# Kernel tuning notes

Hardware: AMD Instinct MI355X
Metric: run time of the kernel (lower is better)

Reference implementation:

```python
import jax, jax.numpy as jnp
import numpy as np

NUM_SPINS = 1024
BATCH = 4096
INPUT_DIM = 2
NUM_HIDDEN = 128
NUM_LAYERS = 1
FIXED_MAG = 0


def setup_inputs() -> dict:
    key = jax.random.key(0)
    ks = jax.random.split(key, 7)
    # spins one-hot encoded, as the module's masking math assumes
    spins = jax.random.randint(ks[0], (NUM_SPINS, BATCH), 0, 2)
    data_in = jax.nn.one_hot(spins, INPUT_DIM, dtype=jnp.float32)
    s = 1.0 / np.sqrt(NUM_HIDDEN)  # torch RNNCell default uniform bound
    W_ih = jax.random.uniform(ks[1], (NUM_HIDDEN, INPUT_DIM), minval=-s, maxval=s, dtype=jnp.float32)
    W_hh = jax.random.uniform(ks[2], (NUM_HIDDEN, NUM_HIDDEN), minval=-s, maxval=s, dtype=jnp.float32)
    b_ih = jax.random.uniform(ks[3], (NUM_HIDDEN,), minval=-s, maxval=s, dtype=jnp.float32)
    b_hh = jax.random.uniform(ks[4], (NUM_HIDDEN,), minval=-s, maxval=s, dtype=jnp.float32)
    W_lin = jax.random.uniform(ks[5], (INPUT_DIM, NUM_HIDDEN), minval=-s, maxval=s, dtype=jnp.float32)
    b_lin = jax.random.uniform(ks[6], (INPUT_DIM,), minval=-s, maxval=s, dtype=jnp.float32)
    return {"data_in": data_in, "W_ih": W_ih, "W_hh": W_hh,
            "b_ih": b_ih, "b_hh": b_hh, "W_lin": W_lin, "b_lin": b_lin}


def reference(data_in, W_ih, W_hh, b_ih, b_hh, W_lin, b_lin):
    S, B, I = data_in.shape
    dt = data_in.dtype
    # input sequence shifted by one spin, first input is init_state [1,0]
    init_state = jnp.array([1.0, 0.0], dtype=dt)
    data = jnp.concatenate([jnp.broadcast_to(init_state, (1, B, I)), data_in[:-1]], axis=0)

    def step(h, x):
        for _ in range(NUM_LAYERS):  # source re-applies the SAME cell num_layers times
            h = jnp.tanh(x @ W_ih.T + b_ih + h @ W_hh.T + b_hh)
        probs = jax.nn.softmax(h @ W_lin.T + b_lin, axis=-1)
        return h, probs

    h0 = jnp.zeros((B, NUM_HIDDEN), dtype=dt)
    _, state_probs = jax.lax.scan(step, h0, data)  # [S, B, I]

    # conditional masking from fixed magnetization
    half = S // 2
    thresh_up = half + (S % 2) + FIXED_MAG // 2
    thresh_down = half - FIXED_MAG // 2
    cum_up = jnp.cumsum(data_in[:, :, 0], axis=0)    # [S, B]
    cum_down = jnp.cumsum(data_in[:, :, 1], axis=0)  # [S, B]
    down_guar = jnp.array([0.0, 1.0], dtype=dt)
    up_guar = jnp.array([1.0, 0.0], dtype=dt)
    mask_up = (cum_up[:-1] >= thresh_up)[..., None]      # for spins 1..S-1
    mask_down = (cum_down[:-1] >= thresh_down)[..., None]
    corr = jnp.where(mask_up, down_guar, state_probs[1:])
    corr = jnp.where(mask_down, up_guar, corr)
    return jnp.concatenate([state_probs[:1], corr], axis=0)
```

## Files before the change

kernel.cpp:

```cpp
#include <hip/hip_runtime.h>

#define NS 1024
#define NB 4096
#define NH 128
#define RB 16
#define NT 512

typedef __attribute__((ext_vector_type(8))) short short8;
typedef __attribute__((ext_vector_type(4))) float f32x4;

__device__ __forceinline__ short f2bf(float x) {
    unsigned u = __builtin_bit_cast(unsigned, x);
    u = (u + 0x7FFFu + ((u >> 16) & 1u)) >> 16;
    return (short)u;
}
__device__ __forceinline__ float vexp2(float x) {
    float r;
    asm("v_exp_f32 %0, %1" : "=v"(r) : "v"(x));
    return r;
}

#define BARRIER() asm volatile("s_waitcnt lgkmcnt(0)\n\ts_barrier" ::: "memory")

__global__ __launch_bounds__(NT, 1)
void pwf_kernel(const float* __restrict__ data_in,
                const float* __restrict__ W_ih,
                const float* __restrict__ W_hh,
                const float* __restrict__ b_ih,
                const float* __restrict__ b_hh,
                const float* __restrict__ W_lin,
                const float* __restrict__ b_lin,
                float* __restrict__ out)
{
    __shared__ __align__(16) short hlds[2][RB * NH];
    __shared__ unsigned selm[2];
    __shared__ uint2    msk[4];

    const int tid = threadIdx.x;
    const int w   = tid >> 6;
    const int l   = tid & 63;
    const int g   = l >> 4;
    const int b   = l & 15;
    const int b0  = blockIdx.x * RB;

    const float TL2E = 2.8853900817779268f;
    const float L2E  = 1.4426950408889634f;

    const int hrow = w * 16 + b;
    short8 afrag[4];
    #pragma unroll
    for (int kb = 0; kb < 4; ++kb) {
        const float* src = W_hh + hrow * NH + kb * 32 + g * 8;
        short8 v;
        #pragma unroll
        for (int i = 0; i < 8; ++i) v[i] = f2bf(TL2E * src[i]);
        afrag[kb] = v;
    }
    short8 lfrag[4];
    #pragma unroll
    for (int kb = 0; kb < 4; ++kb) {
        short8 v;
        #pragma unroll
        for (int i = 0; i < 8; ++i) {
            const int k = kb * 32 + g * 8 + i;
            v[i] = (b == 0) ? f2bf(L2E * (W_lin[NH + k] - W_lin[k])) : (short)0;
        }
        lfrag[kb] = v;
    }

    float cv0[4], cv1[4];
    #pragma unroll
    for (int r = 0; r < 4; ++r) {
        const int hid = w * 16 + 4 * g + r;
        const float cb = b_ih[hid] + b_hh[hid];
        cv0[r] = TL2E * (W_ih[hid * 2 + 0] + cb);
        cv1[r] = TL2E * (W_ih[hid * 2 + 1] + cb);
    }
    const float blD = L2E * (b_lin[1] - b_lin[0]);

    int aoff[4];
    #pragma unroll
    for (int kb = 0; kb < 4; ++kb)
        aoff[kb] = b * NH + ((kb * 32 + g * 8 + 8 * b) & 127);
    const int woffs = b * NH + ((w * 16 + 4 * g + 8 * b) & 127);

    ((uint4*)hlds)[tid] = make_uint4(0u, 0u, 0u, 0u);
    if (tid == 0) { selm[0] = 0u; msk[0] = make_uint2(0u, 0u); }
    int cntup = 0, cntdn = 0;
    const int rr = (l < RB) ? l : (RB - 1);
    float suA = 0.0f, suB = 0.0f;
    if (w == 7) {
        suA = data_in[(size_t)(b0 + rr) * 2];
        suB = data_in[((size_t)NB + b0 + rr) * 2];
    }
    float ediff = 0.0f;
    unsigned eum = 0u, edm = 0u;
    BARRIER();

#define STEP(T, P, SU)                                                         \
    {                                                                          \
        const short* hr = hlds[P];                                             \
        short* hw = hlds[(P) ^ 1];                                             \
        const unsigned sel = selm[P];                                          \
        const short8 h0 = *(const short8*)&hr[aoff[0]];                        \
        const short8 h1 = *(const short8*)&hr[aoff[1]];                        \
        const short8 h2 = *(const short8*)&hr[aoff[2]];                        \
        const short8 h3 = *(const short8*)&hr[aoff[3]];                        \
        if (w == 0 && (T) >= 2 && l < 16) {       \
            float p0 = __builtin_amdgcn_rcpf(1.0f + vexp2(ediff));             \
            float p1 = 1.0f - p0;                                              \
            if ((eum >> l) & 1u) { p0 = 0.0f; p1 = 1.0f; }                     \
            if ((edm >> l) & 1u) { p0 = 1.0f; p1 = 0.0f; }                     \
            *(float2*)&out[((size_t)((T) - 2) * NB + b0 + l) * 2] =            \
                make_float2(p0, p1);                                           \
        }                                                                      \
                           \
        f32x4 zz = {0.f, 0.f, 0.f, 0.f};                                       \
        f32x4 c01 = __builtin_amdgcn_mfma_f32_16x16x32_bf16(afrag[0], h0, zz, 0, 0, 0); \
        c01 = __builtin_amdgcn_mfma_f32_16x16x32_bf16(afrag[1], h1, c01, 0, 0, 0); \
        f32x4 c23 = __builtin_amdgcn_mfma_f32_16x16x32_bf16(afrag[2], h2, zz, 0, 0, 0); \
        c23 = __builtin_amdgcn_mfma_f32_16x16x32_bf16(afrag[3], h3, c23, 0, 0, 0); \
        if (w == 0 && (T) >= 1) {                \
            f32x4 d01 = __builtin_amdgcn_mfma_f32_16x16x32_bf16(lfrag[0], h0, zz, 0, 0, 0); \
            d01 = __builtin_amdgcn_mfma_f32_16x16x32_bf16(lfrag[1], h1, d01, 0, 0, 0); \
            f32x4 d23 = __builtin_amdgcn_mfma_f32_16x16x32_bf16(lfrag[2], h2, zz, 0, 0, 0); \
            d23 = __builtin_amdgcn_mfma_f32_16x16x32_bf16(lfrag[3], h3, d23, 0, 0, 0); \
            ediff = d01[0] + d23[0] + blD;     \
            const uint2 mm = msk[((T) - 1) & 3];                               \
            eum = mm.x; edm = mm.y;                                            \
        }                                                                      \
        const unsigned sb = (sel >> b) & 1u;                                   \
        float hn[4];                                                           \
        _Pragma("unroll")                                                      \
        for (int r = 0; r < 4; ++r) {                                          \
            const float cv = sb ? cv1[r] : cv0[r];                             \
            const float e  = vexp2(c01[r] + c23[r] + cv);                      \
            hn[r] = fmaf(__builtin_amdgcn_rcpf(e + 1.0f), -2.0f, 1.0f);        \
        }                                                                      \
        unsigned pk01, pk23;                                                   \
        asm("v_cvt_pk_bf16_f32 %0, %1, %2" : "=v"(pk01) : "v"(hn[0]), "v"(hn[1])); \
        asm("v_cvt_pk_bf16_f32 %0, %1, %2" : "=v"(pk23) : "v"(hn[2]), "v"(hn[3])); \
        *(uint2*)&hw[woffs] = make_uint2(pk01, pk23);    \
        if (w == 7) {         \
            const int isup = ((SU) > 0.5f) ? 1 : 0;                            \
            cntup += isup; cntdn += 1 - isup;                                  \
            const unsigned long long bs = __ballot(l < RB && isup == 0);       \
            const unsigned long long bu = __ballot(l < RB && cntup >= NS / 2); \
            const unsigned long long bd = __ballot(l < RB && cntdn >= NS / 2); \
            if (l == 0) {                                                      \
                selm[(P) ^ 1] = (unsigned)bs & 0xFFFFu;                        \
                msk[((T) + 1) & 3] =                                           \
                    make_uint2((unsigned)bu & 0xFFFFu, (unsigned)bd & 0xFFFFu);\
            }                                                                  \
            const int tn = ((T) + 2 < NS) ? (T) + 2 : NS - 1;                  \
            (SU) = data_in[((size_t)tn * NB + b0 + rr) * 2];                   \
        }                                                                      \
        BARRIER();                                                             \
    }

    for (int t = 0; t < NS; t += 2) {
        STEP(t, 0, suA)
        STEP(t + 1, 1, suB)
    }

    if (w == 0) {
        if (l < 16) {
            float p0 = __builtin_amdgcn_rcpf(1.0f + vexp2(ediff));
            float p1 = 1.0f - p0;
            if ((eum >> l) & 1u) { p0 = 0.0f; p1 = 1.0f; }
            if ((edm >> l) & 1u) { p0 = 1.0f; p1 = 0.0f; }
            *(float2*)&out[((size_t)(NS - 2) * NB + b0 + l) * 2] =
                make_float2(p0, p1);
        }
        const short* hr = hlds[0];
        const short8 h0 = *(const short8*)&hr[aoff[0]];
        const short8 h1 = *(const short8*)&hr[aoff[1]];
        const short8 h2 = *(const short8*)&hr[aoff[2]];
        const short8 h3 = *(const short8*)&hr[aoff[3]];
        f32x4 zz = {0.f, 0.f, 0.f, 0.f};
        f32x4 d01 = __builtin_amdgcn_mfma_f32_16x16x32_bf16(lfrag[0], h0, zz, 0, 0, 0);
        d01 = __builtin_amdgcn_mfma_f32_16x16x32_bf16(lfrag[1], h1, d01, 0, 0, 0);
        f32x4 d23 = __builtin_amdgcn_mfma_f32_16x16x32_bf16(lfrag[2], h2, zz, 0, 0, 0);
        d23 = __builtin_amdgcn_mfma_f32_16x16x32_bf16(lfrag[3], h3, d23, 0, 0, 0);
        const float fdiff = d01[0] + d23[0] + blD;
        const uint2 mm = msk[(NS - 1) & 3];
        if (l < 16) {
            float p0 = __builtin_amdgcn_rcpf(1.0f + vexp2(fdiff));
            float p1 = 1.0f - p0;
            if ((mm.x >> l) & 1u) { p0 = 0.0f; p1 = 1.0f; }
            if ((mm.y >> l) & 1u) { p0 = 1.0f; p1 = 0.0f; }
            *(float2*)&out[((size_t)(NS - 1) * NB + b0 + l) * 2] =
                make_float2(p0, p1);
        }
    }
}

extern "C" void kernel_launch(void* const* d_in, const int* in_sizes, int n_in,
                              void* d_out, int out_size, void* d_ws, size_t ws_size,
                              hipStream_t stream) {
    const float* data_in = (const float*)d_in[0];
    const float* W_ih    = (const float*)d_in[1];
    const float* W_hh    = (const float*)d_in[2];
    const float* b_ih    = (const float*)d_in[3];
    const float* b_hh    = (const float*)d_in[4];
    const float* W_lin   = (const float*)d_in[5];
    const float* b_lin   = (const float*)d_in[6];
    float* out = (float*)d_out;

    dim3 grid(NB / RB);
    dim3 block(NT);
    pwf_kernel<<<grid, block, 0, stream>>>(data_in, W_ih, W_hh, b_ih, b_hh,
                                           W_lin, b_lin, out);
}
```

Before: 415.5 us.

## Halve batch rows per block and compute masks per-thread, removing LDS mask broadcast

Each block now handles 8 batch rows with 4 waves, and each wave computes two 16-row hidden tiles (X and Y halves) instead of one. This doubles the grid to 512 blocks and allows two blocks per CU. The magnetization counters and input-select bit are now tracked redundantly in every thread, which removes the LDS selm/msk broadcasts and the ballots. The output wave rotates across blocks and raises its priority while writing. In exchange, half of every MFMA is wasted because the 16-wide batch dimension is padded with duplicate rows, and each wave does twice the MFMA work per step.

```diff
diff --git a/kernel.cpp b/kernel.cpp
--- a/kernel.cpp
+++ b/kernel.cpp
@@ -3,8 +3,9 @@
 #define NS 1024
 #define NB 4096
 #define NH 128
-#define RB 16
-#define NT 512
+#define RB 8
+#define NT 256
+#define HLF (NS / 2)
 
 typedef __attribute__((ext_vector_type(8))) short short8;
 typedef __attribute__((ext_vector_type(4))) float f32x4;
@@ -22,7 +23,7 @@
 
 #define BARRIER() asm volatile("s_waitcnt lgkmcnt(0)\n\ts_barrier" ::: "memory")
 
-__global__ __launch_bounds__(NT, 1)
+__global__ __launch_bounds__(NT, 2)
 void pwf_kernel(const float* __restrict__ data_in,
                 const float* __restrict__ W_ih,
                 const float* __restrict__ W_hh,
@@ -33,28 +34,30 @@
                 float* __restrict__ out)
 {
     __shared__ __align__(16) short hlds[2][RB * NH];
-    __shared__ unsigned selm[2];
-    __shared__ uint2    msk[4];
 
     const int tid = threadIdx.x;
     const int w   = tid >> 6;
     const int l   = tid & 63;
     const int g   = l >> 4;
     const int b   = l & 15;
+    const int br  = b & 7;
     const int b0  = blockIdx.x * RB;
+    const int LW  = blockIdx.x & 3;
 
     const float TL2E = 2.8853900817779268f;
     const float L2E  = 1.4426950408889634f;
 
-    const int hrow = w * 16 + b;
-    short8 afrag[4];
+    const int hrX = w * 16 + b;
+    const int hrY = hrX + 64;
+    short8 aX[4], aY[4];
     #pragma unroll
     for (int kb = 0; kb < 4; ++kb) {
-        const float* src = W_hh + hrow * NH + kb * 32 + g * 8;
-        short8 v;
+        const float* sx = W_hh + hrX * NH + kb * 32 + g * 8;
+        const float* sy = W_hh + hrY * NH + kb * 32 + g * 8;
+        short8 vx, vy;
         #pragma unroll
-        for (int i = 0; i < 8; ++i) v[i] = f2bf(TL2E * src[i]);
-        afrag[kb] = v;
+        for (int i = 0; i < 8; ++i) { vx[i] = f2bf(TL2E * sx[i]); vy[i] = f2bf(TL2E * sy[i]); }
+        aX[kb] = vx; aY[kb] = vy;
     }
     short8 lfrag[4];
     #pragma unroll
@@ -68,93 +71,103 @@
         lfrag[kb] = v;
     }
 
-    float cv0[4], cv1[4];
+    float cvX0[4], cvX1[4], cvY0[4], cvY1[4];
     #pragma unroll
     for (int r = 0; r < 4; ++r) {
-        const int hid = w * 16 + 4 * g + r;
-        const float cb = b_ih[hid] + b_hh[hid];
-        cv0[r] = TL2E * (W_ih[hid * 2 + 0] + cb);
-        cv1[r] = TL2E * (W_ih[hid * 2 + 1] + cb);
+        const int hx = w * 16 + 4 * g + r;
+        const int hy = hx + 64;
+        const float cbx = b_ih[hx] + b_hh[hx];
+        const float cby = b_ih[hy] + b_hh[hy];
+        cvX0[r] = TL2E * (W_ih[hx * 2 + 0] + cbx);
+        cvX1[r] = TL2E * (W_ih[hx * 2 + 1] + cbx);
+        cvY0[r] = TL2E * (W_ih[hy * 2 + 0] + cby);
+        cvY1[r] = TL2E * (W_ih[hy * 2 + 1] + cby);
     }
     const float blD = L2E * (b_lin[1] - b_lin[0]);
 
     int aoff[4];
     #pragma unroll
     for (int kb = 0; kb < 4; ++kb)
-        aoff[kb] = b * NH + ((kb * 32 + g * 8 + 8 * b) & 127);
-    const int woffs = b * NH + ((w * 16 + 4 * g + 8 * b) & 127);
+        aoff[kb] = br * NH + ((kb * 32 + g * 8 + 8 * br) & 127);
+    const int woffX = br * NH + ((w * 16 + 4 * g + 8 * br) & 127);
+    const int woffY = br * NH + ((w * 16 + 64 + 4 * g + 8 * br) & 127);
 
     ((uint4*)hlds)[tid] = make_uint4(0u, 0u, 0u, 0u);
-    if (tid == 0) { selm[0] = 0u; msk[0] = make_uint2(0u, 0u); }
     int cntup = 0, cntdn = 0;
-    const int rr = (l < RB) ? l : (RB - 1);
-    float suA = 0.0f, suB = 0.0f;
-    if (w == 7) {
-        suA = data_in[(size_t)(b0 + rr) * 2];
-        suB = data_in[((size_t)NB + b0 + rr) * 2];
-    }
+    int selp = 0;
+    int ump = 0, dmp = 0;
+    float suA = data_in[(size_t)(b0 + br) * 2];
+    float suB = data_in[((size_t)NB + b0 + br) * 2];
     float ediff = 0.0f;
-    unsigned eum = 0u, edm = 0u;
+    int eum = 0, edm = 0;
     BARRIER();
 
 #define STEP(T, P, SU)                                                         \
     {                                                                          \
         const short* hr = hlds[P];                                             \
         short* hw = hlds[(P) ^ 1];                                             \
-        const unsigned sel = selm[P];                                          \
         const short8 h0 = *(const short8*)&hr[aoff[0]];                        \
         const short8 h1 = *(const short8*)&hr[aoff[1]];                        \
         const short8 h2 = *(const short8*)&hr[aoff[2]];                        \
         const short8 h3 = *(const short8*)&hr[aoff[3]];                        \
-        if (w == 0 && (T) >= 2 && l < 16) {       \
-            float p0 = __builtin_amdgcn_rcpf(1.0f + vexp2(ediff));             \
-            float p1 = 1.0f - p0;                                              \
-            if ((eum >> l) & 1u) { p0 = 0.0f; p1 = 1.0f; }                     \
-            if ((edm >> l) & 1u) { p0 = 1.0f; p1 = 0.0f; }                     \
-            *(float2*)&out[((size_t)((T) - 2) * NB + b0 + l) * 2] =            \
-                make_float2(p0, p1);                                           \
-        }                                                                      \
-                           \
+        if (w == LW) {                                                         \
+            __builtin_amdgcn_s_setprio(1);                                     \
+            if ((T) >= 2 && l < 8) {              \
+                float p0 = __builtin_amdgcn_rcpf(1.0f + vexp2(ediff));         \
+                float p1 = 1.0f - p0;                                          \
+                if (eum) { p0 = 0.0f; p1 = 1.0f; }                             \
+                if (edm) { p0 = 1.0f; p1 = 0.0f; }         \
+                *(float2*)&out[((size_t)((T) - 2) * NB + b0 + l) * 2] =        \
+                    make_float2(p0, p1);                                       \
+            }                                                                  \
+        }                                                                      \
+                \
         f32x4 zz = {0.f, 0.f, 0.f, 0.f};                                       \
-        f32x4 c01 = __builtin_amdgcn_mfma_f32_16x16x32_bf16(afrag[0], h0, zz, 0, 0, 0); \
-        c01 = __builtin_amdgcn_mfma_f32_16x16x32_bf16(afrag[1], h1, c01, 0, 0, 0); \
-        f32x4 c23 = __builtin_amdgcn_mfma_f32_16x16x32_bf16(afrag[2], h2, zz, 0, 0, 0); \
-        c23 = __builtin_amdgcn_mfma_f32_16x16x32_bf16(afrag[3], h3, c23, 0, 0, 0); \
-        if (w == 0 && (T) >= 1) {                \
+        f32x4 cX01 = __builtin_amdgcn_mfma_f32_16x16x32_bf16(aX[0], h0, zz, 0, 0, 0); \
+        cX01 = __builtin_amdgcn_mfma_f32_16x16x32_bf16(aX[1], h1, cX01, 0, 0, 0); \
+        f32x4 cX23 = __builtin_amdgcn_mfma_f32_16x16x32_bf16(aX[2], h2, zz, 0, 0, 0); \
+        cX23 = __builtin_amdgcn_mfma_f32_16x16x32_bf16(aX[3], h3, cX23, 0, 0, 0); \
+        f32x4 cY01 = __builtin_amdgcn_mfma_f32_16x16x32_bf16(aY[0], h0, zz, 0, 0, 0); \
+        cY01 = __builtin_amdgcn_mfma_f32_16x16x32_bf16(aY[1], h1, cY01, 0, 0, 0); \
+        f32x4 cY23 = __builtin_amdgcn_mfma_f32_16x16x32_bf16(aY[2], h2, zz, 0, 0, 0); \
+        cY23 = __builtin_amdgcn_mfma_f32_16x16x32_bf16(aY[3], h3, cY23, 0, 0, 0); \
+        if (w == LW && (T) >= 1) {               \
             f32x4 d01 = __builtin_amdgcn_mfma_f32_16x16x32_bf16(lfrag[0], h0, zz, 0, 0, 0); \
             d01 = __builtin_amdgcn_mfma_f32_16x16x32_bf16(lfrag[1], h1, d01, 0, 0, 0); \
             f32x4 d23 = __builtin_amdgcn_mfma_f32_16x16x32_bf16(lfrag[2], h2, zz, 0, 0, 0); \
             d23 = __builtin_amdgcn_mfma_f32_16x16x32_bf16(lfrag[3], h3, d23, 0, 0, 0); \
-            ediff = d01[0] + d23[0] + blD;     \
-            const uint2 mm = msk[((T) - 1) & 3];                               \
-            eum = mm.x; edm = mm.y;                                            \
-        }                                                                      \
-        const unsigned sb = (sel >> b) & 1u;                                   \
-        float hn[4];                                                           \
+            ediff = d01[0] + d23[0] + blD;            \
+            eum = ump; edm = dmp;                      \
+        }                                                                      \
+        ump = (cntup >= HLF);        \
+        dmp = (cntdn >= HLF);                                                  \
+        float hnX[4], hnY[4];                                                  \
         _Pragma("unroll")                                                      \
         for (int r = 0; r < 4; ++r) {                                          \
-            const float cv = sb ? cv1[r] : cv0[r];                             \
-            const float e  = vexp2(c01[r] + c23[r] + cv);                      \
-            hn[r] = fmaf(__builtin_amdgcn_rcpf(e + 1.0f), -2.0f, 1.0f);        \
-        }                                                                      \
-        unsigned pk01, pk23;                                                   \
-        asm("v_cvt_pk_bf16_f32 %0, %1, %2" : "=v"(pk01) : "v"(hn[0]), "v"(hn[1])); \
-        asm("v_cvt_pk_bf16_f32 %0, %1, %2" : "=v"(pk23) : "v"(hn[2]), "v"(hn[3])); \
-        *(uint2*)&hw[woffs] = make_uint2(pk01, pk23);    \
-        if (w == 7) {         \
+            const float cvx = selp ? cvX1[r] : cvX0[r];                        \
+            const float cvy = selp ? cvY1[r] : cvY0[r];                        \
+            const float ex = vexp2(cX01[r] + cX23[r] + cvx);                   \
+            const float ey = vexp2(cY01[r] + cY23[r] + cvy);                   \
+            hnX[r] = fmaf(__builtin_amdgcn_rcpf(ex + 1.0f), -2.0f, 1.0f);      \
+            hnY[r] = fmaf(__builtin_amdgcn_rcpf(ey + 1.0f), -2.0f, 1.0f);      \
+        }                                                                      \
+        {                              \
             const int isup = ((SU) > 0.5f) ? 1 : 0;                            \
             cntup += isup; cntdn += 1 - isup;                                  \
-            const unsigned long long bs = __ballot(l < RB && isup == 0);       \
-            const unsigned long long bu = __ballot(l < RB && cntup >= NS / 2); \
-            const unsigned long long bd = __ballot(l < RB && cntdn >= NS / 2); \
-            if (l == 0) {                                                      \
-                selm[(P) ^ 1] = (unsigned)bs & 0xFFFFu;                        \
-                msk[((T) + 1) & 3] =                                           \
-                    make_uint2((unsigned)bu & 0xFFFFu, (unsigned)bd & 0xFFFFu);\
-            }                                                                  \
+            selp = 1 - isup;                                                   \
             const int tn = ((T) + 2 < NS) ? (T) + 2 : NS - 1;                  \
-            (SU) = data_in[((size_t)tn * NB + b0 + rr) * 2];                   \
-        }                                                                      \
+            (SU) = data_in[((size_t)tn * NB + b0 + br) * 2];                   \
+        }                                                                      \
+        if (b < 8) {                                                           \
+            unsigned pX01, pX23, pY01, pY23;                                   \
+            asm("v_cvt_pk_bf16_f32 %0, %1, %2" : "=v"(pX01) : "v"(hnX[0]), "v"(hnX[1])); \
+            asm("v_cvt_pk_bf16_f32 %0, %1, %2" : "=v"(pX23) : "v"(hnX[2]), "v"(hnX[3])); \
+            asm("v_cvt_pk_bf16_f32 %0, %1, %2" : "=v"(pY01) : "v"(hnY[0]), "v"(hnY[1])); \
+            asm("v_cvt_pk_bf16_f32 %0, %1, %2" : "=v"(pY23) : "v"(hnY[2]), "v"(hnY[3])); \
+            *(uint2*)&hw[woffX] = make_uint2(pX01, pX23);                      \
+            *(uint2*)&hw[woffY] = make_uint2(pY01, pY23);                      \
+        }                                                                      \
+        if (w == LW) __builtin_amdgcn_s_setprio(0);                            \
         BARRIER();                                                             \
     }
 
@@ -163,12 +176,12 @@
         STEP(t + 1, 1, suB)
     }
 
-    if (w == 0) {
-        if (l < 16) {
+    if (w == LW) {
+        if (l < 8) {
             float p0 = __builtin_amdgcn_rcpf(1.0f + vexp2(ediff));
             float p1 = 1.0f - p0;
-            if ((eum >> l) & 1u) { p0 = 0.0f; p1 = 1.0f; }
-            if ((edm >> l) & 1u) { p0 = 1.0f; p1 = 0.0f; }
+            if (eum) { p0 = 0.0f; p1 = 1.0f; }
+            if (edm) { p0 = 1.0f; p1 = 0.0f; }
             *(float2*)&out[((size_t)(NS - 2) * NB + b0 + l) * 2] =
                 make_float2(p0, p1);
         }
@@ -183,12 +196,11 @@
         f32x4 d23 = __builtin_amdgcn_mfma_f32_16x16x32_bf16(lfrag[2], h2, zz, 0, 0, 0);
         d23 = __builtin_amdgcn_mfma_f32_16x16x32_bf16(lfrag[3], h3, d23, 0, 0, 0);
         const float fdiff = d01[0] + d23[0] + blD;
-        const uint2 mm = msk[(NS - 1) & 3];
-        if (l < 16) {
+        if (l < 8) {
             float p0 = __builtin_amdgcn_rcpf(1.0f + vexp2(fdiff));
             float p1 = 1.0f - p0;
-            if ((mm.x >> l) & 1u) { p0 = 0.0f; p1 = 1.0f; }
-            if ((mm.y >> l) & 1u) { p0 = 1.0f; p1 = 0.0f; }
+            if (ump) { p0 = 0.0f; p1 = 1.0f; }
+            if (dmp) { p0 = 1.0f; p1 = 0.0f; }
             *(float2*)&out[((size_t)(NS - 1) * NB + b0 + l) * 2] =
                 make_float2(p0, p1);
         }
```

Result: slower. 532.6 us (+28.2%).

## Run each 16-row batch tile in a single wavefront, keeping hidden state in registers

Applied to the files above, without the earlier changes.

Switches from eight cooperating wavefronts per block, which exchanged the hidden state through LDS with a barrier every step, to one 64-lane wavefront per 16 batch rows. That wavefront holds all of W_hh as bf16 fragments and runs 32 MFMAs per step. The MFMA output layout is repacked directly into the next step's B-operand fragments in registers. The output logit is now a scalar dot product reduced with cross-lane shuffles instead of extra MFMAs. This removes LDS traffic and block barriers, but serialises all hidden units onto one wave, raises register pressure, and leaves only 256 single-wave blocks to fill the GPU.

```diff
diff --git a/kernel.cpp b/kernel.cpp
--- a/kernel.cpp
+++ b/kernel.cpp
@@ -3,11 +3,11 @@
 #define NS 1024
 #define NB 4096
 #define NH 128
-#define RB 16
-#define NT 512
+#define HLF 512
 
 typedef __attribute__((ext_vector_type(8))) short short8;
 typedef __attribute__((ext_vector_type(4))) float f32x4;
+typedef __attribute__((ext_vector_type(4))) unsigned uint32x4;
 
 __device__ __forceinline__ short f2bf(float x) {
     unsigned u = __builtin_bit_cast(unsigned, x);
@@ -20,9 +20,7 @@
     return r;
 }
 
-#define BARRIER() asm volatile("s_waitcnt lgkmcnt(0)\n\ts_barrier" ::: "memory")
-
-__global__ __launch_bounds__(NT, 1)
+__global__ __launch_bounds__(64, 1)
 void pwf_kernel(const float* __restrict__ data_in,
                 const float* __restrict__ W_ih,
                 const float* __restrict__ W_hh,
@@ -32,166 +30,119 @@
                 const float* __restrict__ b_lin,
                 float* __restrict__ out)
 {
-    __shared__ __align__(16) short hlds[2][RB * NH];
-    __shared__ unsigned selm[2];
-    __shared__ uint2    msk[4];
-
-    const int tid = threadIdx.x;
-    const int w   = tid >> 6;
-    const int l   = tid & 63;
-    const int g   = l >> 4;
-    const int b   = l & 15;
-    const int b0  = blockIdx.x * RB;
+    const int l  = threadIdx.x;
+    const int g  = l >> 4;
+    const int b  = l & 15;
+    const int b0 = blockIdx.x * 16;
 
     const float TL2E = 2.8853900817779268f;
     const float L2E  = 1.4426950408889634f;
 
-    const int hrow = w * 16 + b;
-    short8 afrag[4];
+    short8 afr[8][4];
     #pragma unroll
-    for (int kb = 0; kb < 4; ++kb) {
-        const float* src = W_hh + hrow * NH + kb * 32 + g * 8;
-        short8 v;
+    for (int T = 0; T < 8; ++T) {
+        const float* wr = W_hh + (size_t)(16 * T + b) * NH;
         #pragma unroll
-        for (int i = 0; i < 8; ++i) v[i] = f2bf(TL2E * src[i]);
-        afrag[kb] = v;
+        for (int kb = 0; kb < 4; ++kb) {
+            const float* p = wr + 32 * kb + 4 * g;
+            const float4 f0 = *(const float4*)(p);
+            const float4 f1 = *(const float4*)(p + 16);
+            short8 v;
+            v[0] = f2bf(TL2E * f0.x); v[1] = f2bf(TL2E * f0.y);
+            v[2] = f2bf(TL2E * f0.z); v[3] = f2bf(TL2E * f0.w);
+            v[4] = f2bf(TL2E * f1.x); v[5] = f2bf(TL2E * f1.y);
+            v[6] = f2bf(TL2E * f1.z); v[7] = f2bf(TL2E * f1.w);
+            afr[T][kb] = v;
+        }
     }
-    short8 lfrag[4];
+    float cv0[8][4], cv1[8][4], wdf[8][4];
     #pragma unroll
-    for (int kb = 0; kb < 4; ++kb) {
-        short8 v;
+    for (int T = 0; T < 8; ++T) {
         #pragma unroll
-        for (int i = 0; i < 8; ++i) {
-            const int k = kb * 32 + g * 8 + i;
-            v[i] = (b == 0) ? f2bf(L2E * (W_lin[NH + k] - W_lin[k])) : (short)0;
+        for (int r = 0; r < 4; ++r) {
+            const int i = 16 * T + 4 * g + r;
+            const float cb = b_ih[i] + b_hh[i];
+            cv0[T][r] = TL2E * (W_ih[2 * i + 0] + cb);
+            cv1[T][r] = TL2E * (W_ih[2 * i + 1] + cb);
+            wdf[T][r] = L2E * (W_lin[NH + i] - W_lin[i]);
         }
-        lfrag[kb] = v;
-    }
-
-    float cv0[4], cv1[4];
-    #pragma unroll
-    for (int r = 0; r < 4; ++r) {
-        const int hid = w * 16 + 4 * g + r;
-        const float cb = b_ih[hid] + b_hh[hid];
-        cv0[r] = TL2E * (W_ih[hid * 2 + 0] + cb);
-        cv1[r] = TL2E * (W_ih[hid * 2 + 1] + cb);
     }
     const float blD = L2E * (b_lin[1] - b_lin[0]);
 
-    int aoff[4];
-    #pragma unroll
-    for (int kb = 0; kb < 4; ++kb)
-        aoff[kb] = b * NH + ((kb * 32 + g * 8 + 8 * b) & 127);
-    const int woffs = b * NH + ((w * 16 + 4 * g + 8 * b) & 127);
+    short8 frag0 = {0,0,0,0,0,0,0,0}, frag1 = frag0, frag2 = frag0, frag3 = frag0;
+    int   cntup = 0, cntdn = 0, sel = 0;
+    int   eum = 0, edm = 0;
+    float pdiff = 0.0f;
+    float suA = data_in[(size_t)(b0 + b) * 2];
+    float suB = data_in[((size_t)NB + b0 + b) * 2];
 
-    ((uint4*)hlds)[tid] = make_uint4(0u, 0u, 0u, 0u);
-    if (tid == 0) { selm[0] = 0u; msk[0] = make_uint2(0u, 0u); }
-    int cntup = 0, cntdn = 0;
-    const int rr = (l < RB) ? l : (RB - 1);
-    float suA = 0.0f, suB = 0.0f;
-    if (w == 7) {
-        suA = data_in[(size_t)(b0 + rr) * 2];
-        suB = data_in[((size_t)NB + b0 + rr) * 2];
-    }
-    float ediff = 0.0f;
-    unsigned eum = 0u, edm = 0u;
-    BARRIER();
-
-#define STEP(T, P, SU)                                                         \
+#define STEP(T, SU)                                                            \
     {                                                                          \
-        const short* hr = hlds[P];                                             \
-        short* hw = hlds[(P) ^ 1];                                             \
-        const unsigned sel = selm[P];                                          \
-        const short8 h0 = *(const short8*)&hr[aoff[0]];                        \
-        const short8 h1 = *(const short8*)&hr[aoff[1]];                        \
-        const short8 h2 = *(const short8*)&hr[aoff[2]];                        \
-        const short8 h3 = *(const short8*)&hr[aoff[3]];                        \
-        if (w == 0 && (T) >= 2 && l < 16) {       \
-            float p0 = __builtin_amdgcn_rcpf(1.0f + vexp2(ediff));             \
+        if ((T) >= 1 && l < 16) {           \
+            const float ex = vexp2(pdiff);                                     \
+            float p0 = __builtin_amdgcn_rcpf(1.0f + ex);                       \
             float p1 = 1.0f - p0;                                              \
-            if ((eum >> l) & 1u) { p0 = 0.0f; p1 = 1.0f; }                     \
-            if ((edm >> l) & 1u) { p0 = 1.0f; p1 = 0.0f; }                     \
-            *(float2*)&out[((size_t)((T) - 2) * NB + b0 + l) * 2] =            \
+            if (eum) { p0 = 0.0f; p1 = 1.0f; }                                 \
+            if (edm) { p0 = 1.0f; p1 = 0.0f; }          \
+            *(float2*)&out[((size_t)((T) - 1) * NB + b0 + b) * 2] =            \
                 make_float2(p0, p1);                                           \
         }                                                                      \
-                           \
-        f32x4 zz = {0.f, 0.f, 0.f, 0.f};                                       \
-        f32x4 c01 = __builtin_amdgcn_mfma_f32_16x16x32_bf16(afrag[0], h0, zz, 0, 0, 0); \
-        c01 = __builtin_amdgcn_mfma_f32_16x16x32_bf16(afrag[1], h1, c01, 0, 0, 0); \
-        f32x4 c23 = __builtin_amdgcn_mfma_f32_16x16x32_bf16(afrag[2], h2, zz, 0, 0, 0); \
-        c23 = __builtin_amdgcn_mfma_f32_16x16x32_bf16(afrag[3], h3, c23, 0, 0, 0); \
-        if (w == 0 && (T) >= 1) {                \
-            f32x4 d01 = __builtin_amdgcn_mfma_f32_16x16x32_bf16(lfrag[0], h0, zz, 0, 0, 0); \
-            d01 = __builtin_amdgcn_mfma_f32_16x16x32_bf16(lfrag[1], h1, d01, 0, 0, 0); \
-            f32x4 d23 = __builtin_amdgcn_mfma_f32_16x16x32_bf16(lfrag[2], h2, zz, 0, 0, 0); \
-            d23 = __builtin_amdgcn_mfma_f32_16x16x32_bf16(lfrag[3], h3, d23, 0, 0, 0); \
-            ediff = d01[0] + d23[0] + blD;     \
-            const uint2 mm = msk[((T) - 1) & 3];                               \
-            eum = mm.x; edm = mm.y;                                            \
+        const int umc = (cntup >= HLF);            \
+        const int dmc = (cntdn >= HLF);                                        \
+           \
+        f32x4 acc[8];                                                          \
+        _Pragma("unroll")                                                      \
+        for (int T2 = 0; T2 < 8; ++T2) {                                       \
+            f32x4 c = {0.f, 0.f, 0.f, 0.f};                                    \
+            c = __builtin_amdgcn_mfma_f32_16x16x32_bf16(afr[T2][0], frag0, c, 0, 0, 0); \
+            c = __builtin_amdgcn_mfma_f32_16x16x32_bf16(afr[T2][1], frag1, c, 0, 0, 0); \
+            c = __builtin_amdgcn_mfma_f32_16x16x32_bf16(afr[T2][2], frag2, c, 0, 0, 0); \
+            c = __builtin_amdgcn_mfma_f32_16x16x32_bf16(afr[T2][3], frag3, c, 0, 0, 0); \
+            acc[T2] = c;                                                       \
         }                                                                      \
-        const unsigned sb = (sel >> b) & 1u;                                   \
-        float hn[4];                                                           \
+                                             \
+        float ldp = 0.0f;                                                      \
+        unsigned pka[8], pkb[8];                                               \
         _Pragma("unroll")                                                      \
-        for (int r = 0; r < 4; ++r) {                                          \
-            const float cv = sb ? cv1[r] : cv0[r];                             \
-            const float e  = vexp2(c01[r] + c23[r] + cv);                      \
-            hn[r] = fmaf(__builtin_amdgcn_rcpf(e + 1.0f), -2.0f, 1.0f);        \
+        for (int T2 = 0; T2 < 8; ++T2) {                                       \
+            float hn[4];                                                       \
+            _Pragma("unroll")                                                  \
+            for (int r = 0; r < 4; ++r) {                                      \
+                const float cv = sel ? cv1[T2][r] : cv0[T2][r];                \
+                const float e  = vexp2(acc[T2][r] + cv);                       \
+                hn[r] = fmaf(__builtin_amdgcn_rcpf(e + 1.0f), -2.0f, 1.0f);    \
+                ldp   = fmaf(wdf[T2][r], hn[r], ldp);                          \
+            }                                                                  \
+            asm("v_cvt_pk_bf16_f32 %0, %1, %2" : "=v"(pka[T2]) : "v"(hn[0]), "v"(hn[1])); \
+            asm("v_cvt_pk_bf16_f32 %0, %1, %2" : "=v"(pkb[T2]) : "v"(hn[2]), "v"(hn[3])); \
         }                                                                      \
-        unsigned pk01, pk23;                                                   \
-        asm("v_cvt_pk_bf16_f32 %0, %1, %2" : "=v"(pk01) : "v"(hn[0]), "v"(hn[1])); \
-        asm("v_cvt_pk_bf16_f32 %0, %1, %2" : "=v"(pk23) : "v"(hn[2]), "v"(hn[3])); \
-        *(uint2*)&hw[woffs] = make_uint2(pk01, pk23);    \
-        if (w == 7) {         \
-            const int isup = ((SU) > 0.5f) ? 1 : 0;                            \
-            cntup += isup; cntdn += 1 - isup;                                  \
-            const unsigned long long bs = __ballot(l < RB && isup == 0);       \
-            const unsigned long long bu = __ballot(l < RB && cntup >= NS / 2); \
-            const unsigned long long bd = __ballot(l < RB && cntdn >= NS / 2); \
-            if (l == 0) {                                                      \
-                selm[(P) ^ 1] = (unsigned)bs & 0xFFFFu;                        \
-                msk[((T) + 1) & 3] =                                           \
-                    make_uint2((unsigned)bu & 0xFFFFu, (unsigned)bd & 0xFFFFu);\
-            }                                                                  \
-            const int tn = ((T) + 2 < NS) ? (T) + 2 : NS - 1;                  \
-            (SU) = data_in[((size_t)tn * NB + b0 + rr) * 2];                   \
-        }                                                                      \
-        BARRIER();                                                             \
+        ldp += __shfl_xor(ldp, 16);     \
+        ldp += __shfl_xor(ldp, 32);                                            \
+        pdiff = ldp + blD;  eum = umc;  edm = dmc;            \
+                     \
+        frag0 = __builtin_bit_cast(short8, (uint32x4){pka[0], pkb[0], pka[1], pkb[1]}); \
+        frag1 = __builtin_bit_cast(short8, (uint32x4){pka[2], pkb[2], pka[3], pkb[3]}); \
+        frag2 = __builtin_bit_cast(short8, (uint32x4){pka[4], pkb[4], pka[5], pkb[5]}); \
+        frag3 = __builtin_bit_cast(short8, (uint32x4){pka[6], pkb[6], pka[7], pkb[7]}); \
+                                        \
+        const int isup = ((SU) > 0.5f) ? 1 : 0;                                \
+        cntup += isup;  cntdn += 1 - isup;  sel = 1 - isup;                    \
+        const int tn = ((T) + 2 < NS) ? (T) + 2 : NS - 1;                      \
+        (SU) = data_in[((size_t)tn * NB + b0 + b) * 2];                        \
     }
 
     for (int t = 0; t < NS; t += 2) {
-        STEP(t, 0, suA)
-        STEP(t + 1, 1, suB)
+        STEP(t, suA)
+        STEP(t + 1, suB)
     }
 
-    if (w == 0) {
-        if (l < 16) {
-            float p0 = __builtin_amdgcn_rcpf(1.0f + vexp2(ediff));
-            float p1 = 1.0f - p0;
-            if ((eum >> l) & 1u) { p0 = 0.0f; p1 = 1.0f; }
-            if ((edm >> l) & 1u) { p0 = 1.0f; p1 = 0.0f; }
-            *(float2*)&out[((size_t)(NS - 2) * NB + b0 + l) * 2] =
-                make_float2(p0, p1);
-        }
-        const short* hr = hlds[0];
-        const short8 h0 = *(const short8*)&hr[aoff[0]];
-        const short8 h1 = *(const short8*)&hr[aoff[1]];
-        const short8 h2 = *(const short8*)&hr[aoff[2]];
-        const short8 h3 = *(const short8*)&hr[aoff[3]];
-        f32x4 zz = {0.f, 0.f, 0.f, 0.f};
-        f32x4 d01 = __builtin_amdgcn_mfma_f32_16x16x32_bf16(lfrag[0], h0, zz, 0, 0, 0);
-        d01 = __builtin_amdgcn_mfma_f32_16x16x32_bf16(lfrag[1], h1, d01, 0, 0, 0);
-        f32x4 d23 = __builtin_amdgcn_mfma_f32_16x16x32_bf16(lfrag[2], h2, zz, 0, 0, 0);
-        d23 = __builtin_amdgcn_mfma_f32_16x16x32_bf16(lfrag[3], h3, d23, 0, 0, 0);
-        const float fdiff = d01[0] + d23[0] + blD;
-        const uint2 mm = msk[(NS - 1) & 3];
-        if (l < 16) {
-            float p0 = __builtin_amdgcn_rcpf(1.0f + vexp2(fdiff));
-            float p1 = 1.0f - p0;
-            if ((mm.x >> l) & 1u) { p0 = 0.0f; p1 = 1.0f; }
-            if ((mm.y >> l) & 1u) { p0 = 1.0f; p1 = 0.0f; }
-            *(float2*)&out[((size_t)(NS - 1) * NB + b0 + l) * 2] =
-                make_float2(p0, p1);
-        }
+    if (l < 16) {
+        const float ex = vexp2(pdiff);
+        float p0 = __builtin_amdgcn_rcpf(1.0f + ex);
+        float p1 = 1.0f - p0;
+        if (eum) { p0 = 0.0f; p1 = 1.0f; }
+        if (edm) { p0 = 1.0f; p1 = 0.0f; }
+        *(float2*)&out[((size_t)(NS - 1) * NB + b0 + b) * 2] = make_float2(p0, p1);
     }
 }
 
@@ -207,8 +158,8 @@
     const float* b_lin   = (const float*)d_in[6];
     float* out = (float*)d_out;
 
-    dim3 grid(NB / RB);
-    dim3 block(NT);
+    dim3 grid(NB / 16);
+    dim3 block(64);
     pwf_kernel<<<grid, block, 0, stream>>>(data_in, W_ih, W_hh, b_ih, b_hh,
                                            W_lin, b_lin, out);
 }
```

Result: slower. 912.4 us (+119.6%).

## Interleave two independent batch groups per block to overlap MFMA and tanh phases

Applied to the files above, without the earlier changes.

Each block now processes 32 batch rows as two independent 16-row recurrences, A and B, in alternating phases. While one group's MFMA matmul is issued, the other group's tanh activation and h store run, so MFMA latency is hidden behind transcendental work. The spin counters and masks move from a single wave plus LDS ballots into per-lane registers. The grid halves to 128 blocks, which may leave many of the 256 CUs idle, and the number of barriers per timestep doubles.

```diff
diff --git a/kernel.cpp b/kernel.cpp
--- a/kernel.cpp
+++ b/kernel.cpp
@@ -3,7 +3,7 @@
 #define NS 1024
 #define NB 4096
 #define NH 128
-#define RB 16
+#define HLF 512
 #define NT 512
 
 typedef __attribute__((ext_vector_type(8))) short short8;
@@ -21,6 +21,8 @@
 }
 
 #define BARRIER() asm volatile("s_waitcnt lgkmcnt(0)\n\ts_barrier" ::: "memory")
+
+#define MFMA __builtin_amdgcn_mfma_f32_16x16x32_bf16
 
 __global__ __launch_bounds__(NT, 1)
 void pwf_kernel(const float* __restrict__ data_in,
@@ -32,16 +34,16 @@
                 const float* __restrict__ b_lin,
                 float* __restrict__ out)
 {
-    __shared__ __align__(16) short hlds[2][RB * NH];
-    __shared__ unsigned selm[2];
-    __shared__ uint2    msk[4];
+    __shared__ __align__(16) short hlds[2][16 * NH];
+    short* const hA = hlds[0];
+    short* const hB = hlds[1];
 
     const int tid = threadIdx.x;
     const int w   = tid >> 6;
     const int l   = tid & 63;
     const int g   = l >> 4;
     const int b   = l & 15;
-    const int b0  = blockIdx.x * RB;
+    const int b0  = blockIdx.x * 32;
 
     const float TL2E = 2.8853900817779268f;
     const float L2E  = 1.4426950408889634f;
@@ -67,7 +69,6 @@
         }
         lfrag[kb] = v;
     }
-
     float cv0[4], cv1[4];
     #pragma unroll
     for (int r = 0; r < 4; ++r) {
@@ -85,112 +86,192 @@
     const int woffs = b * NH + ((w * 16 + 4 * g + 8 * b) & 127);
 
     ((uint4*)hlds)[tid] = make_uint4(0u, 0u, 0u, 0u);
-    if (tid == 0) { selm[0] = 0u; msk[0] = make_uint2(0u, 0u); }
-    int cntup = 0, cntdn = 0;
-    const int rr = (l < RB) ? l : (RB - 1);
-    float suA = 0.0f, suB = 0.0f;
-    if (w == 7) {
-        suA = data_in[(size_t)(b0 + rr) * 2];
-        suB = data_in[((size_t)NB + b0 + rr) * 2];
-    }
-    float ediff = 0.0f;
-    unsigned eum = 0u, edm = 0u;
+    f32x4 accA0 = {0,0,0,0}, accA1 = accA0, accB0 = accA0, accB1 = accA0;
+    int selA = 0, cupA = 0, cdnA = 0, snapUA = 0, snapDA = 0;
+    int selB = 0, cupB = 0, cdnB = 0, snapUB = 0, snapDB = 0;
+    float edfA = 0.f, edfB = 0.f;
+    int eumA = 0, edmA = 0, eumB = 0, edmB = 0;
+    float sA0 = data_in[((size_t)0 * NB + b0 + b) * 2];
+    float sA1 = data_in[((size_t)1 * NB + b0 + b) * 2];
+    float sB0 = data_in[((size_t)0 * NB + b0 + 16 + b) * 2];
+    float sB1 = data_in[((size_t)1 * NB + b0 + 16 + b) * 2];
     BARRIER();
 
-#define STEP(T, P, SU)                                                         \
+#define PHA(T, SBS)                                                            \
     {                                                                          \
-        const short* hr = hlds[P];                                             \
-        short* hw = hlds[(P) ^ 1];                                             \
-        const unsigned sel = selm[P];                                          \
-        const short8 h0 = *(const short8*)&hr[aoff[0]];                        \
-        const short8 h1 = *(const short8*)&hr[aoff[1]];                        \
-        const short8 h2 = *(const short8*)&hr[aoff[2]];                        \
-        const short8 h3 = *(const short8*)&hr[aoff[3]];                        \
-        if (w == 0 && (T) >= 2 && l < 16) {       \
-            float p0 = __builtin_amdgcn_rcpf(1.0f + vexp2(ediff));             \
-            float p1 = 1.0f - p0;                                              \
-            if ((eum >> l) & 1u) { p0 = 0.0f; p1 = 1.0f; }                     \
-            if ((edm >> l) & 1u) { p0 = 1.0f; p1 = 0.0f; }                     \
-            *(float2*)&out[((size_t)((T) - 2) * NB + b0 + l) * 2] =            \
-                make_float2(p0, p1);                                           \
-        }                                                                      \
-                           \
+        const short8 h0 = *(const short8*)&hA[aoff[0]];                        \
+        const short8 h1 = *(const short8*)&hA[aoff[1]];                        \
+        const short8 h2 = *(const short8*)&hA[aoff[2]];                        \
+        const short8 h3 = *(const short8*)&hA[aoff[3]];                        \
+        if (w == 0) {                                                          \
+            if ((T) >= 2 && l < 16) {                                          \
+                float p0 = __builtin_amdgcn_rcpf(1.0f + vexp2(edfA));          \
+                float p1 = 1.0f - p0;                                          \
+                if (eumA) { p0 = 0.0f; p1 = 1.0f; }                            \
+                if (edmA) { p0 = 1.0f; p1 = 0.0f; }                            \
+                *(float2*)&out[((size_t)((T) - 2) * NB + b0 + l) * 2] =        \
+                    make_float2(p0, p1);                                       \
+            }                                                                  \
+            if ((T) >= 1) {                                                    \
+                f32x4 zl = {0.f, 0.f, 0.f, 0.f};                               \
+                f32x4 d01 = MFMA(lfrag[0], h0, zl, 0, 0, 0);                   \
+                d01 = MFMA(lfrag[1], h1, d01, 0, 0, 0);                        \
+                f32x4 d23 = MFMA(lfrag[2], h2, zl, 0, 0, 0);                   \
+                d23 = MFMA(lfrag[3], h3, d23, 0, 0, 0);                        \
+                edfA = d01[0] + d23[0] + blD;                                  \
+                eumA = snapUA; edmA = snapDA;                                  \
+            }                                                                  \
+        }                                                                      \
         f32x4 zz = {0.f, 0.f, 0.f, 0.f};                                       \
-        f32x4 c01 = __builtin_amdgcn_mfma_f32_16x16x32_bf16(afrag[0], h0, zz, 0, 0, 0); \
-        c01 = __builtin_amdgcn_mfma_f32_16x16x32_bf16(afrag[1], h1, c01, 0, 0, 0); \
-        f32x4 c23 = __builtin_amdgcn_mfma_f32_16x16x32_bf16(afrag[2], h2, zz, 0, 0, 0); \
-        c23 = __builtin_amdgcn_mfma_f32_16x16x32_bf16(afrag[3], h3, c23, 0, 0, 0); \
-        if (w == 0 && (T) >= 1) {                \
-            f32x4 d01 = __builtin_amdgcn_mfma_f32_16x16x32_bf16(lfrag[0], h0, zz, 0, 0, 0); \
-            d01 = __builtin_amdgcn_mfma_f32_16x16x32_bf16(lfrag[1], h1, d01, 0, 0, 0); \
-            f32x4 d23 = __builtin_amdgcn_mfma_f32_16x16x32_bf16(lfrag[2], h2, zz, 0, 0, 0); \
-            d23 = __builtin_amdgcn_mfma_f32_16x16x32_bf16(lfrag[3], h3, d23, 0, 0, 0); \
-            ediff = d01[0] + d23[0] + blD;     \
-            const uint2 mm = msk[((T) - 1) & 3];                               \
-            eum = mm.x; edm = mm.y;                                            \
-        }                                                                      \
-        const unsigned sb = (sel >> b) & 1u;                                   \
-        float hn[4];                                                           \
-        _Pragma("unroll")                                                      \
-        for (int r = 0; r < 4; ++r) {                                          \
-            const float cv = sb ? cv1[r] : cv0[r];                             \
-            const float e  = vexp2(c01[r] + c23[r] + cv);                      \
-            hn[r] = fmaf(__builtin_amdgcn_rcpf(e + 1.0f), -2.0f, 1.0f);        \
-        }                                                                      \
-        unsigned pk01, pk23;                                                   \
-        asm("v_cvt_pk_bf16_f32 %0, %1, %2" : "=v"(pk01) : "v"(hn[0]), "v"(hn[1])); \
-        asm("v_cvt_pk_bf16_f32 %0, %1, %2" : "=v"(pk23) : "v"(hn[2]), "v"(hn[3])); \
-        *(uint2*)&hw[woffs] = make_uint2(pk01, pk23);    \
-        if (w == 7) {         \
-            const int isup = ((SU) > 0.5f) ? 1 : 0;                            \
-            cntup += isup; cntdn += 1 - isup;                                  \
-            const unsigned long long bs = __ballot(l < RB && isup == 0);       \
-            const unsigned long long bu = __ballot(l < RB && cntup >= NS / 2); \
-            const unsigned long long bd = __ballot(l < RB && cntdn >= NS / 2); \
-            if (l == 0) {                                                      \
-                selm[(P) ^ 1] = (unsigned)bs & 0xFFFFu;                        \
-                msk[((T) + 1) & 3] =                                           \
-                    make_uint2((unsigned)bu & 0xFFFFu, (unsigned)bd & 0xFFFFu);\
-            }                                                                  \
+        accA0 = MFMA(afrag[0], h0, zz, 0, 0, 0);                               \
+        accA0 = MFMA(afrag[1], h1, accA0, 0, 0, 0);                            \
+        accA1 = MFMA(afrag[2], h2, zz, 0, 0, 0);                               \
+        accA1 = MFMA(afrag[3], h3, accA1, 0, 0, 0);                            \
+        if ((T) >= 1) {                               \
+            snapUB = (cupB >= HLF); snapDB = (cdnB >= HLF);                    \
+            float hn[4];                                                       \
+            _Pragma("unroll")                                                  \
+            for (int r = 0; r < 4; ++r) {                                      \
+                const float cv = selB ? cv1[r] : cv0[r];                       \
+                const float e  = vexp2(accB0[r] + accB1[r] + cv);              \
+                hn[r] = fmaf(__builtin_amdgcn_rcpf(e + 1.0f), -2.0f, 1.0f);    \
+            }                                                                  \
+            unsigned pk01, pk23;                                               \
+            asm("v_cvt_pk_bf16_f32 %0, %1, %2" : "=v"(pk01) : "v"(hn[0]), "v"(hn[1])); \
+            asm("v_cvt_pk_bf16_f32 %0, %1, %2" : "=v"(pk23) : "v"(hn[2]), "v"(hn[3])); \
+            *(uint2*)&hB[woffs] = make_uint2(pk01, pk23);                      \
+            const int isup = ((SBS) > 0.5f) ? 1 : 0;           \
+            cupB += isup; cdnB += 1 - isup; selB = 1 - isup;                   \
+            const int tn = ((T) + 1 < NS) ? (T) + 1 : NS - 1;                  \
+            (SBS) = data_in[((size_t)tn * NB + b0 + 16 + b) * 2];              \
+        }                                                                      \
+        BARRIER();                                                             \
+    }
+
+#define PHB(T, SAS)                                                            \
+    {                                                                          \
+        const short8 h0 = *(const short8*)&hB[aoff[0]];                        \
+        const short8 h1 = *(const short8*)&hB[aoff[1]];                        \
+        const short8 h2 = *(const short8*)&hB[aoff[2]];                        \
+        const short8 h3 = *(const short8*)&hB[aoff[3]];                        \
+        if (w == 2) {                                                          \
+            if ((T) >= 2 && l < 16) {                                          \
+                float p0 = __builtin_amdgcn_rcpf(1.0f + vexp2(edfB));          \
+                float p1 = 1.0f - p0;                                          \
+                if (eumB) { p0 = 0.0f; p1 = 1.0f; }                            \
+                if (edmB) { p0 = 1.0f; p1 = 0.0f; }                            \
+                *(float2*)&out[((size_t)((T) - 2) * NB + b0 + 16 + l) * 2] =   \
+                    make_float2(p0, p1);                                       \
+            }                                                                  \
+            if ((T) >= 1) {                                                    \
+                f32x4 zl = {0.f, 0.f, 0.f, 0.f};                               \
+                f32x4 d01 = MFMA(lfrag[0], h0, zl, 0, 0, 0);                   \
+                d01 = MFMA(lfrag[1], h1, d01, 0, 0, 0);                        \
+                f32x4 d23 = MFMA(lfrag[2], h2, zl, 0, 0, 0);                   \
+                d23 = MFMA(lfrag[3], h3, d23, 0, 0, 0);                        \
+                edfB = d01[0] + d23[0] + blD;                                  \
+                eumB = snapUB; edmB = snapDB;                                  \
+            }                                                                  \
+        }                                                                      \
+        f32x4 zz = {0.f, 0.f, 0.f, 0.f};                                       \
+        accB0 = MFMA(afrag[0], h0, zz, 0, 0, 0);                               \
+        accB0 = MFMA(afrag[1], h1, accB0, 0, 0, 0);                            \
+        accB1 = MFMA(afrag[2], h2, zz, 0, 0, 0);                               \
+        accB1 = MFMA(afrag[3], h3, accB1, 0, 0, 0);                            \
+        {                                           \
+            snapUA = (cupA >= HLF); snapDA = (cdnA >= HLF);                    \
+            float hn[4];                                                       \
+            _Pragma("unroll")                                                  \
+            for (int r = 0; r < 4; ++r) {                                      \
+                const float cv = selA ? cv1[r] : cv0[r];                       \
+                const float e  = vexp2(accA0[r] + accA1[r] + cv);              \
+                hn[r] = fmaf(__builtin_amdgcn_rcpf(e + 1.0f), -2.0f, 1.0f);    \
+            }                                                                  \
+            unsigned pk01, pk23;                                               \
+            asm("v_cvt_pk_bf16_f32 %0, %1, %2" : "=v"(pk01) : "v"(hn[0]), "v"(hn[1])); \
+            asm("v_cvt_pk_bf16_f32 %0, %1, %2" : "=v"(pk23) : "v"(hn[2]), "v"(hn[3])); \
+            *(uint2*)&hA[woffs] = make_uint2(pk01, pk23);                      \
+            const int isup = ((SAS) > 0.5f) ? 1 : 0;             \
+            cupA += isup; cdnA += 1 - isup; selA = 1 - isup;                   \
             const int tn = ((T) + 2 < NS) ? (T) + 2 : NS - 1;                  \
-            (SU) = data_in[((size_t)tn * NB + b0 + rr) * 2];                   \
+            (SAS) = data_in[((size_t)tn * NB + b0 + b) * 2];                   \
         }                                                                      \
         BARRIER();                                                             \
     }
 
     for (int t = 0; t < NS; t += 2) {
-        STEP(t, 0, suA)
-        STEP(t + 1, 1, suB)
-    }
+        PHA(t, sB1)
+        PHB(t, sA0)
+        PHA(t + 1, sB0)
+        PHB(t + 1, sA1)
+    }
+
+    {
+        snapUB = (cupB >= HLF); snapDB = (cdnB >= HLF);
+        float hn[4];
+        #pragma unroll
+        for (int r = 0; r < 4; ++r) {
+            const float cv = selB ? cv1[r] : cv0[r];
+            const float e  = vexp2(accB0[r] + accB1[r] + cv);
+            hn[r] = fmaf(__builtin_amdgcn_rcpf(e + 1.0f), -2.0f, 1.0f);
+        }
+        unsigned pk01, pk23;
+        asm("v_cvt_pk_bf16_f32 %0, %1, %2" : "=v"(pk01) : "v"(hn[0]), "v"(hn[1]));
+        asm("v_cvt_pk_bf16_f32 %0, %1, %2" : "=v"(pk23) : "v"(hn[2]), "v"(hn[3]));
+        *(uint2*)&hB[woffs] = make_uint2(pk01, pk23);
+    }
+    BARRIER();
 
     if (w == 0) {
         if (l < 16) {
-            float p0 = __builtin_amdgcn_rcpf(1.0f + vexp2(ediff));
-            float p1 = 1.0f - p0;
-            if ((eum >> l) & 1u) { p0 = 0.0f; p1 = 1.0f; }
-            if ((edm >> l) & 1u) { p0 = 1.0f; p1 = 0.0f; }
-            *(float2*)&out[((size_t)(NS - 2) * NB + b0 + l) * 2] =
-                make_float2(p0, p1);
-        }
-        const short* hr = hlds[0];
-        const short8 h0 = *(const short8*)&hr[aoff[0]];
-        const short8 h1 = *(const short8*)&hr[aoff[1]];
-        const short8 h2 = *(const short8*)&hr[aoff[2]];
-        const short8 h3 = *(const short8*)&hr[aoff[3]];
-        f32x4 zz = {0.f, 0.f, 0.f, 0.f};
-        f32x4 d01 = __builtin_amdgcn_mfma_f32_16x16x32_bf16(lfrag[0], h0, zz, 0, 0, 0);
-        d01 = __builtin_amdgcn_mfma_f32_16x16x32_bf16(lfrag[1], h1, d01, 0, 0, 0);
-        f32x4 d23 = __builtin_amdgcn_mfma_f32_16x16x32_bf16(lfrag[2], h2, zz, 0, 0, 0);
-        d23 = __builtin_amdgcn_mfma_f32_16x16x32_bf16(lfrag[3], h3, d23, 0, 0, 0);
-        const float fdiff = d01[0] + d23[0] + blD;
-        const uint2 mm = msk[(NS - 1) & 3];
-        if (l < 16) {
-            float p0 = __builtin_amdgcn_rcpf(1.0f + vexp2(fdiff));
-            float p1 = 1.0f - p0;
-            if ((mm.x >> l) & 1u) { p0 = 0.0f; p1 = 1.0f; }
-            if ((mm.y >> l) & 1u) { p0 = 1.0f; p1 = 0.0f; }
-            *(float2*)&out[((size_t)(NS - 1) * NB + b0 + l) * 2] =
-                make_float2(p0, p1);
+            float p0 = __builtin_amdgcn_rcpf(1.0f + vexp2(edfA));
+            float p1 = 1.0f - p0;
+            if (eumA) { p0 = 0.0f; p1 = 1.0f; }
+            if (edmA) { p0 = 1.0f; p1 = 0.0f; }
+            *(float2*)&out[((size_t)(NS - 2) * NB + b0 + l) * 2] = make_float2(p0, p1);
+        }
+        const short8 h0 = *(const short8*)&hA[aoff[0]];
+        const short8 h1 = *(const short8*)&hA[aoff[1]];
+        const short8 h2 = *(const short8*)&hA[aoff[2]];
+        const short8 h3 = *(const short8*)&hA[aoff[3]];
+        f32x4 zl = {0.f, 0.f, 0.f, 0.f};
+        f32x4 d01 = MFMA(lfrag[0], h0, zl, 0, 0, 0);
+        d01 = MFMA(lfrag[1], h1, d01, 0, 0, 0);
+        f32x4 d23 = MFMA(lfrag[2], h2, zl, 0, 0, 0);
+        d23 = MFMA(lfrag[3], h3, d23, 0, 0, 0);
+        const float fd = d01[0] + d23[0] + blD;
+        if (l < 16) {
+            float p0 = __builtin_amdgcn_rcpf(1.0f + vexp2(fd));
+            float p1 = 1.0f - p0;
+            if (snapUA) { p0 = 0.0f; p1 = 1.0f; }
+            if (snapDA) { p0 = 1.0f; p1 = 0.0f; }
+            *(float2*)&out[((size_t)(NS - 1) * NB + b0 + l) * 2] = make_float2(p0, p1);
+        }
+    }
+    if (w == 2) {
+        if (l < 16) {
+            float p0 = __builtin_amdgcn_rcpf(1.0f + vexp2(edfB));
+            float p1 = 1.0f - p0;
+            if (eumB) { p0 = 0.0f; p1 = 1.0f; }
+            if (edmB) { p0 = 1.0f; p1 = 0.0f; }
+            *(float2*)&out[((size_t)(NS - 2) * NB + b0 + 16 + l) * 2] = make_float2(p0, p1);
+        }
+        const short8 h0 = *(const short8*)&hB[aoff[0]];
+        const short8 h1 = *(const short8*)&hB[aoff[1]];
+        const short8 h2 = *(const short8*)&hB[aoff[2]];
+        const short8 h3 = *(const short8*)&hB[aoff[3]];
+        f32x4 zl = {0.f, 0.f, 0.f, 0.f};
+        f32x4 d01 = MFMA(lfrag[0], h0, zl, 0, 0, 0);
+        d01 = MFMA(lfrag[1], h1, d01, 0, 0, 0);
+        f32x4 d23 = MFMA(lfrag[2], h2, zl, 0, 0, 0);
+        d23 = MFMA(lfrag[3], h3, d23, 0, 0, 0);
+        const float fd = d01[0] + d23[0] + blD;
+        if (l < 16) {
+            float p0 = __builtin_amdgcn_rcpf(1.0f + vexp2(fd));
+            float p1 = 1.0f - p0;
+            if (snapUB) { p0 = 0.0f; p1 = 1.0f; }
+            if (snapDB) { p0 = 1.0f; p1 = 0.0f; }
+            *(float2*)&out[((size_t)(NS - 1) * NB + b0 + 16 + l) * 2] = make_float2(p0, p1);
         }
     }
 }
@@ -207,7 +288,7 @@
     const float* b_lin   = (const float*)d_in[6];
     float* out = (float*)d_out;
 
-    dim3 grid(NB / RB);
+    dim3 grid(NB / 32);
     dim3 block(NT);
     pwf_kernel<<<grid, block, 0, stream>>>(data_in, W_ih, W_hh, b_ih, b_hh,
                                            W_lin, b_lin, out);
```

After: 733.7 us. +76.6%, slower.
